# Kernel tuning notes

Measured on AMD Instinct MI355X. Metric: run time of the kernel, lower is better.

The kernel has to match this reference:

```python
import jax, jax.numpy as jnp
import numpy as np

EPS = 1e-6
C = 0.01  # global curvature from init_kwargs


def mobius_add(x, y, c):
    # x, y broadcastable [..., d]
    x2 = jnp.sum(x * x, axis=-1, keepdims=True)
    y2 = jnp.sum(y * y, axis=-1, keepdims=True)
    xy = jnp.sum(x * y, axis=-1, keepdims=True)
    num = (1 + 2 * c * xy + c * y2) * x + (1 - c * x2) * y
    den = 1 + 2 * c * xy + (c ** 2) * x2 * y2
    return num / (den + EPS)


def log_map_zero(x, c):
    sqrt_c = jnp.sqrt(c)
    norm = jnp.maximum(jnp.linalg.norm(x, axis=-1, keepdims=True), EPS)
    arg = jnp.minimum(sqrt_c * norm, 1.0 - 1e-5)
    return jnp.arctanh(arg) * x / (sqrt_c * norm)


def exp_map_zero(v, c):
    sqrt_c = jnp.sqrt(c)
    norm = jnp.maximum(jnp.linalg.norm(v, axis=-1, keepdims=True), EPS)
    return jnp.tanh(sqrt_c * norm) * v / (sqrt_c * norm)


def setup_inputs() -> dict:
    key = jax.random.key(0)
    k1, k2, k3, k4, k5, k6, k7 = jax.random.split(key, 7)
    num_entities, d = 20000, 256
    num_rel2 = 512  # num_relations * 2
    B = 1024
    # Poincare-ball embeddings: keep norms well inside radius 1/sqrt(c)=10
    entity_embedding = 0.05 * jax.random.normal(k1, (num_entities, d), dtype=jnp.float32)
    # relation embeddings live in tangent space
    rel_embedding = 0.05 * jax.random.normal(k2, (num_rel2, d), dtype=jnp.float32)
    s = jax.random.randint(k3, (B,), 0, num_entities)
    r = jax.random.randint(k4, (B,), 0, num_rel2)
    o = jax.random.randint(k5, (B,), 0, num_entities)
    triplets = jnp.stack([s, r, o], axis=1).astype(jnp.int64)
    xav = float(np.sqrt(6.0 / (d + d)))
    W_s = jax.random.uniform(k6, (d, d), dtype=jnp.float32, minval=-xav, maxval=xav)
    W_o = jax.random.uniform(k7, (d, d), dtype=jnp.float32, minval=-xav, maxval=xav)
    rel_bias = jnp.zeros((num_rel2,), dtype=jnp.float32)
    return {"entity_embedding": entity_embedding, "rel_embedding": rel_embedding,
            "triplets": triplets, "W_s": W_s, "W_o": W_o, "rel_bias": rel_bias}


def reference(entity_embedding, rel_embedding, triplets, W_s, W_o, rel_bias):
    c = C
    s_emb = entity_embedding[triplets[:, 0]]  # (B, d)
    o_emb = entity_embedding[triplets[:, 2]]  # (B, d)
    # tangent-space linear transforms (MuRP-style), dropout=0 -> identity
    s_tan = log_map_zero(s_emb, c) @ W_s
    o_tan = log_map_zero(o_emb, c) @ W_o
    s_h = exp_map_zero(s_tan, c)
    o_h = exp_map_zero(o_tan, c)
    # Mobius difference query q = (-h_s) (+)_c h_o
    query = mobius_add(-s_h, o_h, c)  # (B, d)
    # relation embeddings mapped from tangent space onto the ball
    rel_h = exp_map_zero(rel_embedding, c)  # (N, d)
    # proxy distance score: -||(-q) (+)_c r||^2 + bias, fully vectorized (B, N, d)
    diff = mobius_add(-query[:, None, :], rel_h[None, :, :], c)
    dist_sq = jnp.sum(diff * diff, axis=-1)  # (B, N)
    scores = -dist_sq + rel_bias[None, :]
    return scores
```

## Files before the change

### kernel.cpp

```cpp
#include <hip/hip_runtime.h>
#include <math.h>

#define EPSF 1e-6f
#define CCF  0.01f
#define SQRT_C 0.1f

typedef __attribute__((ext_vector_type(8))) short bf16x8;
typedef __attribute__((ext_vector_type(4))) float f32x4;

__device__ __forceinline__ float wred(float v) {
#pragma unroll
    for (int o = 32; o > 0; o >>= 1) v += __shfl_xor(v, o, 64);
    return v;
}
__device__ __forceinline__ unsigned f2bf1(float x) {
    unsigned u = __builtin_bit_cast(unsigned, x);
    return (u + 0x7FFFu + ((u >> 16) & 1u)) >> 16;
}
__device__ __forceinline__ uint2 pack4(float4 v) {
    uint2 r;
    r.x = f2bf1(v.x) | (f2bf1(v.y) << 16);
    r.y = f2bf1(v.z) | (f2bf1(v.w) << 16);
    return r;
}

__global__ __launch_bounds__(256) void k1(const float* __restrict__ E,
                                          const int* __restrict__ trip,
                                          const float* __restrict__ rel,
                                          const float* __restrict__ Ws,
                                          const float* __restrict__ Wo,
                                          unsigned short* __restrict__ xs,
                                          unsigned short* __restrict__ relbf,
                                          float* __restrict__ y2,
                                          unsigned short* __restrict__ WT) {
    __shared__ float tile[64][65];
    int blk = blockIdx.x;
    int t = threadIdx.x, w = t >> 6, lane = t & 63;
    if (blk < 128) {
#pragma unroll
        for (int rr = 0; rr < 4; ++rr) {
            int z = blk * 16 + rr * 4 + w;
            int b = z & 1023;
            int col = (z >> 10) ? 2 : 0;
            int idx = trip[b * 3 + col];
            idx = max(0, min(idx, 19999));
            float4 v = *(const float4*)(E + (size_t)idx * 256 + lane * 4);
            float ss = v.x * v.x;
            ss = fmaf(v.y, v.y, ss);
            ss = fmaf(v.z, v.z, ss);
            ss = fmaf(v.w, v.w, ss);
            ss = wred(ss);
            float n = fmaxf(sqrtf(ss), EPSF);
            float arg = fminf(SQRT_C * n, 1.f - 1e-5f);
            float s = atanhf(arg) / (SQRT_C * n);
            v.x *= s; v.y *= s; v.z *= s; v.w *= s;
            *(uint2*)(xs + (size_t)z * 256 + lane * 4) = pack4(v);
        }
    } else if (blk < 144) {
#pragma unroll
        for (int rr = 0; rr < 8; ++rr) {
            int r = (blk - 128) * 32 + rr * 4 + w;
            float4 v = *(const float4*)(rel + (size_t)r * 256 + lane * 4);
            float ss = v.x * v.x;
            ss = fmaf(v.y, v.y, ss);
            ss = fmaf(v.z, v.z, ss);
            ss = fmaf(v.w, v.w, ss);
            ss = wred(ss);
            float n = fmaxf(sqrtf(ss), EPSF);
            float s = tanhf(SQRT_C * n) / (SQRT_C * n);
            v.x *= s; v.y *= s; v.z *= s; v.w *= s;
            *(uint2*)(relbf + (size_t)r * 256 + lane * 4) = pack4(v);
            if (lane == 0) y2[r] = s * s * ss;
        }
    } else {
        int blk2 = blk - 144;
        int mat = blk2 >> 4;
        int tl = blk2 & 15;
        int k0 = (tl >> 2) * 64, n0 = (tl & 3) * 64;
        const float* __restrict__ W = mat ? Wo : Ws;
#pragma unroll 4
        for (int p = 0; p < 16; ++p) {
            int i = p * 4 + w;
            tile[i][lane] = W[(size_t)(k0 + i) * 256 + n0 + lane];
        }
        __syncthreads();
#pragma unroll 4
        for (int p = 0; p < 16; ++p) {
            int n = p * 4 + w;
            WT[(size_t)mat * 65536 + (size_t)(n0 + n) * 256 + k0 + lane] =
                (unsigned short)f2bf1(tile[lane][n]);
        }
    }
}

__global__ __launch_bounds__(256) void k2(const unsigned short* __restrict__ xs,
                                          const unsigned short* __restrict__ WT,
                                          float* __restrict__ T) {
    __shared__ unsigned short Al[32 * 256];
    __shared__ unsigned short Bl[64 * 256];
    int bid = blockIdx.x;
    int M0 = (bid >> 2) * 32, N0 = (bid & 3) * 64;
    int mat = (M0 >= 1024);
    int t = threadIdx.x, w = t >> 6, lane = t & 63;
    int row16 = lane & 15, g = lane >> 4;
    char* Ab = (char*)Al;
    char* Bb = (char*)Bl;
#pragma unroll
    for (int i = 0; i < 4; ++i) {
        int L = i * 256 + t, r = L >> 5, c = L & 31;
        bf16x8 v = *(const bf16x8*)(xs + (size_t)(M0 + r) * 256 + c * 8);
        *(bf16x8*)(Ab + r * 512 + ((c * 16) ^ ((r & 7) << 4))) = v;
    }
#pragma unroll
    for (int i = 0; i < 8; ++i) {
        int L = i * 256 + t, r = L >> 5, c = L & 31;
        bf16x8 v = *(const bf16x8*)(WT + (size_t)mat * 65536 + (size_t)(N0 + r) * 256 + c * 8);
        *(bf16x8*)(Bb + r * 512 + ((c * 16) ^ ((r & 7) << 4))) = v;
    }
    __syncthreads();
    int wm = (w >> 1) * 16, wn = (w & 1) * 32;
    f32x4 acc0 = {0.f, 0.f, 0.f, 0.f};
    f32x4 acc1 = {0.f, 0.f, 0.f, 0.f};
    int mr = wm + row16, n0r = wn + row16, n1r = wn + 16 + row16;
#pragma unroll
    for (int kt = 0; kt < 8; ++kt) {
        bf16x8 a  = *(const bf16x8*)(Ab + mr * 512 + ((kt * 64 + g * 16) ^ ((mr & 7) << 4)));
        bf16x8 b0 = *(const bf16x8*)(Bb + n0r * 512 + ((kt * 64 + g * 16) ^ ((n0r & 7) << 4)));
        bf16x8 b1 = *(const bf16x8*)(Bb + n1r * 512 + ((kt * 64 + g * 16) ^ ((n1r & 7) << 4)));
        acc0 = __builtin_amdgcn_mfma_f32_16x16x32_bf16(a, b0, acc0, 0, 0, 0);
        acc1 = __builtin_amdgcn_mfma_f32_16x16x32_bf16(a, b1, acc1, 0, 0, 0);
    }
#pragma unroll
    for (int i = 0; i < 4; ++i) {
        int m = M0 + wm + g * 4 + i;
        T[(size_t)m * 256 + N0 + wn + row16]      = acc0[i];
        T[(size_t)m * 256 + N0 + wn + 16 + row16] = acc1[i];
    }
}

__global__ __launch_bounds__(512) void k3(const float* __restrict__ T,
                                          unsigned short* __restrict__ qbf,
                                          float* __restrict__ q2) {
    int t = threadIdx.x, w = t >> 6, lane = t & 63;
    int b = blockIdx.x * 8 + w;
    float4 sv = *(const float4*)(T + (size_t)b * 256 + lane * 4);
    float4 ov = *(const float4*)(T + (size_t)(1024 + b) * 256 + lane * 4);
    float sss = sv.x * sv.x, sso = ov.x * ov.x, sdot = sv.x * ov.x;
    sss = fmaf(sv.y, sv.y, sss); sso = fmaf(ov.y, ov.y, sso); sdot = fmaf(sv.y, ov.y, sdot);
    sss = fmaf(sv.z, sv.z, sss); sso = fmaf(ov.z, ov.z, sso); sdot = fmaf(sv.z, ov.z, sdot);
    sss = fmaf(sv.w, sv.w, sss); sso = fmaf(ov.w, ov.w, sso); sdot = fmaf(sv.w, ov.w, sdot);
    sss = wred(sss); sso = wred(sso); sdot = wred(sdot);
    float ns = fmaxf(sqrtf(sss), EPSF);
    float no = fmaxf(sqrtf(sso), EPSF);
    float scs = tanhf(SQRT_C * ns) / (SQRT_C * ns);
    float sco = tanhf(SQRT_C * no) / (SQRT_C * no);
    float x2 = scs * scs * sss;
    float yy2 = sco * sco * sso;
    float xy = -scs * sco * sdot;
    float a1 = 1.f + 2.f * CCF * xy + CCF * yy2;
    float b1 = 1.f - CCF * x2;
    float den = 1.f + 2.f * CCF * xy + CCF * CCF * x2 * yy2 + EPSF;
    float rden = 1.f / den;
    float4 qv;
    qv.x = (a1 * (-scs * sv.x) + b1 * (sco * ov.x)) * rden;
    qv.y = (a1 * (-scs * sv.y) + b1 * (sco * ov.y)) * rden;
    qv.z = (a1 * (-scs * sv.z) + b1 * (sco * ov.z)) * rden;
    qv.w = (a1 * (-scs * sv.w) + b1 * (sco * ov.w)) * rden;
    float qq = qv.x * qv.x;
    qq = fmaf(qv.y, qv.y, qq);
    qq = fmaf(qv.z, qv.z, qq);
    qq = fmaf(qv.w, qv.w, qq);
    qq = wred(qq);
    *(uint2*)(qbf + (size_t)b * 256 + lane * 4) = pack4(qv);
    if (lane == 0) q2[b] = qq;
}

__global__ __launch_bounds__(256) void k4(const unsigned short* __restrict__ qbf,
                                          const unsigned short* __restrict__ relbf,
                                          const float* __restrict__ q2,
                                          const float* __restrict__ y2,
                                          const float* __restrict__ rbias,
                                          float* __restrict__ out) {
    __shared__ unsigned short Al[32 * 256];
    __shared__ unsigned short Bl[64 * 256];
    __shared__ float q2l[32], y2l[64], rbl[64];
    int bid = blockIdx.x;
    int M0 = (bid >> 3) * 32, N0 = (bid & 7) * 64;
    int t = threadIdx.x, w = t >> 6, lane = t & 63;
    int row16 = lane & 15, g = lane >> 4;
    char* Ab = (char*)Al;
    char* Bb = (char*)Bl;
#pragma unroll
    for (int i = 0; i < 4; ++i) {
        int L = i * 256 + t, r = L >> 5, c = L & 31;
        bf16x8 v = *(const bf16x8*)(qbf + (size_t)(M0 + r) * 256 + c * 8);
        *(bf16x8*)(Ab + r * 512 + ((c * 16) ^ ((r & 7) << 4))) = v;
    }
#pragma unroll
    for (int i = 0; i < 8; ++i) {
        int L = i * 256 + t, r = L >> 5, c = L & 31;
        bf16x8 v = *(const bf16x8*)(relbf + (size_t)(N0 + r) * 256 + c * 8);
        *(bf16x8*)(Bb + r * 512 + ((c * 16) ^ ((r & 7) << 4))) = v;
    }
    if (t < 32) q2l[t] = q2[M0 + t];
    else if (t < 96) y2l[t - 32] = y2[N0 + t - 32];
    else if (t < 160) rbl[t - 96] = rbias[N0 + t - 96];
    __syncthreads();
    int wm = (w >> 1) * 16, wn = (w & 1) * 32;
    f32x4 acc0 = {0.f, 0.f, 0.f, 0.f};
    f32x4 acc1 = {0.f, 0.f, 0.f, 0.f};
    int mr = wm + row16, n0r = wn + row16, n1r = wn + 16 + row16;
#pragma unroll
    for (int kt = 0; kt < 8; ++kt) {
        bf16x8 a  = *(const bf16x8*)(Ab + mr * 512 + ((kt * 64 + g * 16) ^ ((mr & 7) << 4)));
        bf16x8 b0 = *(const bf16x8*)(Bb + n0r * 512 + ((kt * 64 + g * 16) ^ ((n0r & 7) << 4)));
        bf16x8 b1 = *(const bf16x8*)(Bb + n1r * 512 + ((kt * 64 + g * 16) ^ ((n1r & 7) << 4)));
        acc0 = __builtin_amdgcn_mfma_f32_16x16x32_bf16(a, b0, acc0, 0, 0, 0);
        acc1 = __builtin_amdgcn_mfma_f32_16x16x32_bf16(a, b1, acc1, 0, 0, 0);
    }
#pragma unroll
    for (int tt = 0; tt < 2; ++tt) {
        int rloc = wn + tt * 16 + row16;
        int r = N0 + rloc;
        f32x4 a = tt ? acc1 : acc0;
        float y2r = y2l[rloc];
        float rb = rbl[rloc];
#pragma unroll
        for (int i = 0; i < 4; ++i) {
            int mloc = wm + g * 4 + i;
            float xy = -a[i];
            float x2 = q2l[mloc];
            float a1 = 1.f + 2.f * CCF * xy + CCF * y2r;
            float b1 = 1.f - CCF * x2;
            float den = 1.f + 2.f * CCF * xy + CCF * CCF * x2 * y2r + EPSF;
            float num2 = a1 * a1 * x2 + 2.f * a1 * b1 * xy + b1 * b1 * y2r;
            out[(size_t)(M0 + mloc) * 512 + r] = -(num2 / (den * den)) + rb;
        }
    }
}

extern "C" void kernel_launch(void* const* d_in, const int* in_sizes, int n_in,
                              void* d_out, int out_size, void* d_ws, size_t ws_size,
                              hipStream_t stream) {
    const float* E = (const float*)d_in[0];
    const float* rel = (const float*)d_in[1];
    const int* trip = (const int*)d_in[2];
    const float* Ws = (const float*)d_in[3];
    const float* Wo = (const float*)d_in[4];
    const float* rbias = (const float*)d_in[5];
    float* out = (float*)d_out;

    char* p = (char*)d_ws;
    unsigned short* xs    = (unsigned short*)p;  p += (size_t)2048 * 256 * 2;
    float*          T     = (float*)p;           p += (size_t)2048 * 256 * 4;
    unsigned short* qbf   = (unsigned short*)p;  p += (size_t)1024 * 256 * 2;
    float*          q2    = (float*)p;           p += 4096;
    unsigned short* relbf = (unsigned short*)p;  p += (size_t)512 * 256 * 2;
    float*          y2    = (float*)p;           p += 2048;
    unsigned short* WT    = (unsigned short*)p;  p += (size_t)2 * 256 * 256 * 2;

    k1<<<176, 256, 0, stream>>>(E, trip, rel, Ws, Wo, xs, relbf, y2, WT);
    k2<<<256, 256, 0, stream>>>(xs, WT, T);
    k3<<<128, 512, 0, stream>>>(T, qbf, q2);
    k4<<<256, 256, 0, stream>>>(qbf, relbf, q2, y2, rbias, out);
}
```

Baseline: 22.26 us.

## Fuse gather/log-map, projection GEMM and Mobius query into one kernel

New measurement: 28.59 us. 28.4% more time.

```diff
diff --git a/kernel.cpp b/kernel.cpp
--- a/kernel.cpp
+++ b/kernel.cpp
@@ -24,42 +24,19 @@
     return r;
 }
 
-__global__ __launch_bounds__(256) void k1(const float* __restrict__ E,
-                                          const int* __restrict__ trip,
-                                          const float* __restrict__ rel,
+__global__ __launch_bounds__(256) void k1(const float* __restrict__ rel,
                                           const float* __restrict__ Ws,
                                           const float* __restrict__ Wo,
-                                          unsigned short* __restrict__ xs,
                                           unsigned short* __restrict__ relbf,
                                           float* __restrict__ y2,
                                           unsigned short* __restrict__ WT) {
     __shared__ float tile[64][65];
     int blk = blockIdx.x;
     int t = threadIdx.x, w = t >> 6, lane = t & 63;
-    if (blk < 128) {
-#pragma unroll
-        for (int rr = 0; rr < 4; ++rr) {
-            int z = blk * 16 + rr * 4 + w;
-            int b = z & 1023;
-            int col = (z >> 10) ? 2 : 0;
-            int idx = trip[b * 3 + col];
-            idx = max(0, min(idx, 19999));
-            float4 v = *(const float4*)(E + (size_t)idx * 256 + lane * 4);
-            float ss = v.x * v.x;
-            ss = fmaf(v.y, v.y, ss);
-            ss = fmaf(v.z, v.z, ss);
-            ss = fmaf(v.w, v.w, ss);
-            ss = wred(ss);
-            float n = fmaxf(sqrtf(ss), EPSF);
-            float arg = fminf(SQRT_C * n, 1.f - 1e-5f);
-            float s = atanhf(arg) / (SQRT_C * n);
-            v.x *= s; v.y *= s; v.z *= s; v.w *= s;
-            *(uint2*)(xs + (size_t)z * 256 + lane * 4) = pack4(v);
-        }
-    } else if (blk < 144) {
+    if (blk < 16) {
 #pragma unroll
         for (int rr = 0; rr < 8; ++rr) {
-            int r = (blk - 128) * 32 + rr * 4 + w;
+            int r = blk * 32 + rr * 4 + w;
             float4 v = *(const float4*)(rel + (size_t)r * 256 + lane * 4);
             float ss = v.x * v.x;
             ss = fmaf(v.y, v.y, ss);
@@ -73,7 +50,7 @@
             if (lane == 0) y2[r] = s * s * ss;
         }
     } else {
-        int blk2 = blk - 144;
+        int blk2 = blk - 16;
         int mat = blk2 >> 4;
         int tl = blk2 & 15;
         int k0 = (tl >> 2) * 64, n0 = (tl & 3) * 64;
@@ -93,86 +70,100 @@
     }
 }
 
-__global__ __launch_bounds__(256) void k2(const unsigned short* __restrict__ xs,
-                                          const unsigned short* __restrict__ WT,
-                                          float* __restrict__ T) {
-    __shared__ unsigned short Al[32 * 256];
-    __shared__ unsigned short Bl[64 * 256];
-    int bid = blockIdx.x;
-    int M0 = (bid >> 2) * 32, N0 = (bid & 3) * 64;
-    int mat = (M0 >= 1024);
-    int t = threadIdx.x, w = t >> 6, lane = t & 63;
+__global__ __launch_bounds__(512) void k23(const float* __restrict__ E,
+                                           const int* __restrict__ trip,
+                                           const unsigned short* __restrict__ WT,
+                                           unsigned short* __restrict__ qbf,
+                                           float* __restrict__ q2) {
+    __shared__ unsigned short Abf[2][16][256];
+    __shared__ float T[32][260];
+
+    int b0 = blockIdx.x * 16;
+    int t = threadIdx.x;
+    int w = t >> 6, lane = t & 63;
     int row16 = lane & 15, g = lane >> 4;
-    char* Ab = (char*)Al;
-    char* Bb = (char*)Bl;
-#pragma unroll
-    for (int i = 0; i < 4; ++i) {
-        int L = i * 256 + t, r = L >> 5, c = L & 31;
-        bf16x8 v = *(const bf16x8*)(xs + (size_t)(M0 + r) * 256 + c * 8);
-        *(bf16x8*)(Ab + r * 512 + ((c * 16) ^ ((r & 7) << 4))) = v;
-    }
-#pragma unroll
-    for (int i = 0; i < 8; ++i) {
-        int L = i * 256 + t, r = L >> 5, c = L & 31;
-        bf16x8 v = *(const bf16x8*)(WT + (size_t)mat * 65536 + (size_t)(N0 + r) * 256 + c * 8);
-        *(bf16x8*)(Bb + r * 512 + ((c * 16) ^ ((r & 7) << 4))) = v;
+
+#pragma unroll
+    for (int j = 0; j < 4; ++j) {
+        int pr = w * 4 + j;
+        int half = pr >> 4, r = pr & 15;
+        int col = half ? 2 : 0;
+        int idx = trip[(b0 + r) * 3 + col];
+        idx = max(0, min(idx, 19999));
+        float4 v = *(const float4*)(E + (size_t)idx * 256 + lane * 4);
+        float ss = v.x * v.x;
+        ss = fmaf(v.y, v.y, ss);
+        ss = fmaf(v.z, v.z, ss);
+        ss = fmaf(v.w, v.w, ss);
+        ss = wred(ss);
+        float n = fmaxf(sqrtf(ss), EPSF);
+        float arg = fminf(SQRT_C * n, 1.f - 1e-5f);
+        float s = atanhf(arg) / (SQRT_C * n);
+        v.x *= s; v.y *= s; v.z *= s; v.w *= s;
+        char* base = (char*)&Abf[half][0][0];
+        *(uint2*)(base + r * 512 + ((lane * 8) ^ ((r & 7) << 4))) = pack4(v);
     }
     __syncthreads();
-    int wm = (w >> 1) * 16, wn = (w & 1) * 32;
-    f32x4 acc0 = {0.f, 0.f, 0.f, 0.f};
-    f32x4 acc1 = {0.f, 0.f, 0.f, 0.f};
-    int mr = wm + row16, n0r = wn + row16, n1r = wn + 16 + row16;
-#pragma unroll
-    for (int kt = 0; kt < 8; ++kt) {
-        bf16x8 a  = *(const bf16x8*)(Ab + mr * 512 + ((kt * 64 + g * 16) ^ ((mr & 7) << 4)));
-        bf16x8 b0 = *(const bf16x8*)(Bb + n0r * 512 + ((kt * 64 + g * 16) ^ ((n0r & 7) << 4)));
-        bf16x8 b1 = *(const bf16x8*)(Bb + n1r * 512 + ((kt * 64 + g * 16) ^ ((n1r & 7) << 4)));
-        acc0 = __builtin_amdgcn_mfma_f32_16x16x32_bf16(a, b0, acc0, 0, 0, 0);
-        acc1 = __builtin_amdgcn_mfma_f32_16x16x32_bf16(a, b1, acc1, 0, 0, 0);
-    }
-#pragma unroll
-    for (int i = 0; i < 4; ++i) {
-        int m = M0 + wm + g * 4 + i;
-        T[(size_t)m * 256 + N0 + wn + row16]      = acc0[i];
-        T[(size_t)m * 256 + N0 + wn + 16 + row16] = acc1[i];
-    }
-}
-
-__global__ __launch_bounds__(512) void k3(const float* __restrict__ T,
-                                          unsigned short* __restrict__ qbf,
-                                          float* __restrict__ q2) {
-    int t = threadIdx.x, w = t >> 6, lane = t & 63;
-    int b = blockIdx.x * 8 + w;
-    float4 sv = *(const float4*)(T + (size_t)b * 256 + lane * 4);
-    float4 ov = *(const float4*)(T + (size_t)(1024 + b) * 256 + lane * 4);
-    float sss = sv.x * sv.x, sso = ov.x * ov.x, sdot = sv.x * ov.x;
-    sss = fmaf(sv.y, sv.y, sss); sso = fmaf(ov.y, ov.y, sso); sdot = fmaf(sv.y, ov.y, sdot);
-    sss = fmaf(sv.z, sv.z, sss); sso = fmaf(ov.z, ov.z, sso); sdot = fmaf(sv.z, ov.z, sdot);
-    sss = fmaf(sv.w, sv.w, sss); sso = fmaf(ov.w, ov.w, sso); sdot = fmaf(sv.w, ov.w, sdot);
-    sss = wred(sss); sso = wred(sso); sdot = wred(sdot);
-    float ns = fmaxf(sqrtf(sss), EPSF);
-    float no = fmaxf(sqrtf(sso), EPSF);
-    float scs = tanhf(SQRT_C * ns) / (SQRT_C * ns);
-    float sco = tanhf(SQRT_C * no) / (SQRT_C * no);
-    float x2 = scs * scs * sss;
-    float yy2 = sco * sco * sso;
-    float xy = -scs * sco * sdot;
-    float a1 = 1.f + 2.f * CCF * xy + CCF * yy2;
-    float b1 = 1.f - CCF * x2;
-    float den = 1.f + 2.f * CCF * xy + CCF * CCF * x2 * yy2 + EPSF;
-    float rden = 1.f / den;
-    float4 qv;
-    qv.x = (a1 * (-scs * sv.x) + b1 * (sco * ov.x)) * rden;
-    qv.y = (a1 * (-scs * sv.y) + b1 * (sco * ov.y)) * rden;
-    qv.z = (a1 * (-scs * sv.z) + b1 * (sco * ov.z)) * rden;
-    qv.w = (a1 * (-scs * sv.w) + b1 * (sco * ov.w)) * rden;
-    float qq = qv.x * qv.x;
-    qq = fmaf(qv.y, qv.y, qq);
-    qq = fmaf(qv.z, qv.z, qq);
-    qq = fmaf(qv.w, qv.w, qq);
-    qq = wred(qq);
-    *(uint2*)(qbf + (size_t)b * 256 + lane * 4) = pack4(qv);
-    if (lane == 0) q2[b] = qq;
+
+    {
+        int mat = w >> 2;
+        int nc = (w & 3) * 64;
+        const char* Abase = (const char*)&Abf[mat][0][0];
+        const unsigned short* Wb = WT + (size_t)mat * 65536;
+        bf16x8 af[8];
+#pragma unroll
+        for (int kt = 0; kt < 8; ++kt)
+            af[kt] = *(const bf16x8*)(Abase + row16 * 512 + ((kt * 64 + g * 16) ^ ((row16 & 7) << 4)));
+#pragma unroll
+        for (int tile = 0; tile < 4; ++tile) {
+            int nr = nc + tile * 16 + row16;
+            f32x4 acc = {0.f, 0.f, 0.f, 0.f};
+#pragma unroll
+            for (int kt = 0; kt < 8; ++kt) {
+                bf16x8 b = *(const bf16x8*)(Wb + (size_t)nr * 256 + kt * 32 + g * 8);
+                acc = __builtin_amdgcn_mfma_f32_16x16x32_bf16(af[kt], b, acc, 0, 0, 0);
+            }
+#pragma unroll
+            for (int i = 0; i < 4; ++i)
+                T[mat * 16 + g * 4 + i][nc + tile * 16 + row16] = acc[i];
+        }
+    }
+    __syncthreads();
+
+#pragma unroll
+    for (int j = 0; j < 2; ++j) {
+        int p = w * 2 + j;
+        float4 sv = *(const float4*)&T[p][lane * 4];
+        float4 ov = *(const float4*)&T[16 + p][lane * 4];
+        float sss = sv.x * sv.x, sso = ov.x * ov.x, sdot = sv.x * ov.x;
+        sss = fmaf(sv.y, sv.y, sss); sso = fmaf(ov.y, ov.y, sso); sdot = fmaf(sv.y, ov.y, sdot);
+        sss = fmaf(sv.z, sv.z, sss); sso = fmaf(ov.z, ov.z, sso); sdot = fmaf(sv.z, ov.z, sdot);
+        sss = fmaf(sv.w, sv.w, sss); sso = fmaf(ov.w, ov.w, sso); sdot = fmaf(sv.w, ov.w, sdot);
+        sss = wred(sss); sso = wred(sso); sdot = wred(sdot);
+        float ns = fmaxf(sqrtf(sss), EPSF);
+        float no = fmaxf(sqrtf(sso), EPSF);
+        float scs = tanhf(SQRT_C * ns) / (SQRT_C * ns);
+        float sco = tanhf(SQRT_C * no) / (SQRT_C * no);
+        float x2 = scs * scs * sss;
+        float yy2 = sco * sco * sso;
+        float xy = -scs * sco * sdot;
+        float a1 = 1.f + 2.f * CCF * xy + CCF * yy2;
+        float b1 = 1.f - CCF * x2;
+        float den = 1.f + 2.f * CCF * xy + CCF * CCF * x2 * yy2 + EPSF;
+        float rden = 1.f / den;
+        float4 qv;
+        qv.x = (a1 * (-scs * sv.x) + b1 * (sco * ov.x)) * rden;
+        qv.y = (a1 * (-scs * sv.y) + b1 * (sco * ov.y)) * rden;
+        qv.z = (a1 * (-scs * sv.z) + b1 * (sco * ov.z)) * rden;
+        qv.w = (a1 * (-scs * sv.w) + b1 * (sco * ov.w)) * rden;
+        float qq = qv.x * qv.x;
+        qq = fmaf(qv.y, qv.y, qq);
+        qq = fmaf(qv.z, qv.z, qq);
+        qq = fmaf(qv.w, qv.w, qq);
+        qq = wred(qq);
+        *(uint2*)(qbf + (size_t)(b0 + p) * 256 + lane * 4) = pack4(qv);
+        if (lane == 0) q2[b0 + p] = qq;
+    }
 }
 
 __global__ __launch_bounds__(256) void k4(const unsigned short* __restrict__ qbf,
@@ -251,16 +242,13 @@
     float* out = (float*)d_out;
 
     char* p = (char*)d_ws;
-    unsigned short* xs    = (unsigned short*)p;  p += (size_t)2048 * 256 * 2;
-    float*          T     = (float*)p;           p += (size_t)2048 * 256 * 4;
     unsigned short* qbf   = (unsigned short*)p;  p += (size_t)1024 * 256 * 2;
     float*          q2    = (float*)p;           p += 4096;
     unsigned short* relbf = (unsigned short*)p;  p += (size_t)512 * 256 * 2;
     float*          y2    = (float*)p;           p += 2048;
     unsigned short* WT    = (unsigned short*)p;  p += (size_t)2 * 256 * 256 * 2;
 
-    k1<<<176, 256, 0, stream>>>(E, trip, rel, Ws, Wo, xs, relbf, y2, WT);
-    k2<<<256, 256, 0, stream>>>(xs, WT, T);
-    k3<<<128, 512, 0, stream>>>(T, qbf, q2);
+    k1<<<48, 256, 0, stream>>>(rel, Ws, Wo, relbf, y2, WT);
+    k23<<<64, 512, 0, stream>>>(E, trip, WT, qbf, q2);
     k4<<<256, 256, 0, stream>>>(qbf, relbf, q2, y2, rbias, out);
 }
```
